# Kernel tuning notes

Hardware: AMD Instinct MI355X
Metric: run time of the kernel (lower is better)

## Reference

```python
import jax, jax.numpy as jnp
import numpy as np

C = 256
CI = C // 2  # inter_channels


def conv1x1(x, w, b):
    # x: [B,C,H,W], w: [O,C], b: [O] -> [B,O,H,W]
    return jnp.einsum('bchw,oc->bohw', x, w) + b[None, :, None, None]


def setup_inputs() -> dict:
    key = jax.random.key(0)
    ks = jax.random.split(key, 9)
    B, H, W = 8, 56, 56
    s = 0.02
    return {
        'x': jax.random.normal(ks[0], (B, C, H, W), dtype=jnp.float32),
        'g_w': jax.random.normal(ks[1], (CI, C), dtype=jnp.float32) * s,
        'g_b': jax.random.normal(ks[2], (CI,), dtype=jnp.float32) * s,
        'theta_w': jax.random.normal(ks[3], (CI, C), dtype=jnp.float32) * s,
        'theta_b': jax.random.normal(ks[4], (CI,), dtype=jnp.float32) * s,
        'phi_w': jax.random.normal(ks[5], (CI, C), dtype=jnp.float32) * s,
        'phi_b': jax.random.normal(ks[6], (CI,), dtype=jnp.float32) * s,
        'W_w': jax.random.normal(ks[7], (C, CI), dtype=jnp.float32) * s,
        'W_b': jax.random.normal(ks[8], (C,), dtype=jnp.float32) * s,
    }


def reference(x, g_w, g_b, theta_w, theta_b, phi_w, phi_b, W_w, W_b):
    B, Cc, H, Wd = x.shape
    N = H * Wd
    g_x = conv1x1(x, g_w, g_b).reshape(B, CI, N).transpose(0, 2, 1)        # [B,N,CI]
    theta_x = conv1x1(x, theta_w, theta_b).reshape(B, CI, N).transpose(0, 2, 1)  # [B,N,CI]
    phi_x = conv1x1(x, phi_w, phi_b).reshape(B, CI, N)                     # [B,CI,N]
    f = jnp.einsum('bnc,bcm->bnm', theta_x, phi_x)                         # [B,N,N]
    attn = jax.nn.softmax(f, axis=-1)
    y = jnp.einsum('bnm,bmc->bnc', attn, g_x)                              # [B,N,CI]
    y = y.transpose(0, 2, 1).reshape(B, CI, H, Wd)                         # [B,CI,H,W]
    z = conv1x1(y, W_w, W_b) + x
    return z
```

## Files before the change

### kernel.cpp

```cpp
#include <hip/hip_runtime.h>

#define NB 8
#define C 256
#define CI 128
#define NPIX 3136
#define NT 64
#define NTILES 49
#define NG 25
#define NSPLIT 4
#define LOG2E 1.44269504f

typedef unsigned short u16;
typedef unsigned int u32;
typedef __bf16 bf16x8 __attribute__((ext_vector_type(8)));
typedef float f32x4 __attribute__((ext_vector_type(4)));
typedef float f32x16 __attribute__((ext_vector_type(16)));

static __device__ __forceinline__ u16 f2b(float f) {
  union { float f; u32 u; } v; v.f = f;
  u32 r = v.u + 0x7FFFu + ((v.u >> 16) & 1u);
  return (u16)(r >> 16);
}
static __device__ __forceinline__ float b2f(u16 v) {
  union { u32 u; float f; } x; x.u = ((u32)v) << 16; return x.f;
}
static __device__ __forceinline__ u32 cvtpk(float lo, float hi) {
  u32 r;
  asm("v_cvt_pk_bf16_f32 %0, %1, %2" : "=v"(r) : "v"(lo), "v"(hi));
  return r;
}
static __device__ __forceinline__ void swap32(u32& x, u32& y) {
  asm("v_permlane32_swap_b32 %0, %1" : "+v"(x), "+v"(y));
}
static __device__ __forceinline__ void gl16(const void* g, void* l) {
  __builtin_amdgcn_global_load_lds(
      (const __attribute__((address_space(1))) u32*)g,
      (__attribute__((address_space(3))) u32*)l, 16, 0, 0);
}

__global__ __launch_bounds__(256) void k0_convert(
    const float* __restrict__ g_w, const float* __restrict__ th_w,
    const float* __restrict__ ph_w, const float* __restrict__ W_w,
    u16* __restrict__ wcat, u16* __restrict__ Wbf) {
  int i = blockIdx.x * 256 + threadIdx.x;
  if (i < 98304) {
    int o = i >> 8, c = i & 255;
    float v = (o < 128) ? g_w[o * 256 + c]
            : (o < 256) ? th_w[(o - 128) * 256 + c] * LOG2E
                        : ph_w[(o - 256) * 256 + c];
    wcat[i] = f2b(v);
  } else {
    int j = i - 98304;
    Wbf[j] = f2b(W_w[j]);
  }
}

__global__ __launch_bounds__(256) void k1_proj(
    const float* __restrict__ x, const float* __restrict__ g_b,
    const float* __restrict__ th_b, const float* __restrict__ ph_b,
    const u16* __restrict__ wcat, u16* __restrict__ thO,
    u16* __restrict__ phO, u16* __restrict__ gO) {
  __shared__ __align__(16) u16 xT[64 * 256];
  char* xTb = reinterpret_cast<char*>(xT);
  int tid = threadIdx.x;
  int b = blockIdx.x / NTILES, nt = blockIdx.x % NTILES;
  int n0 = nt * NT;
  const float* xb = x + (size_t)b * C * NPIX;
  {
    int c0 = tid >> 4, nq = tid & 15;
    for (int k = 0; k < 16; ++k) {
      int c = c0 + 16 * k;
      float4 xv = *reinterpret_cast<const float4*>(xb + (size_t)c * NPIX + n0 + 4 * nq);
      float vals[4] = {xv.x, xv.y, xv.z, xv.w};
#pragma unroll
      for (int j = 0; j < 4; ++j) {
        int row = 4 * nq + j;
        int off = row * 512 + ((((c >> 3) ^ (row & 7))) << 4) + (c & 7) * 2;
        *reinterpret_cast<u16*>(xTb + off) = f2b(vals[j]);
      }
    }
  }
  __syncthreads();
  int wave = tid >> 6, lane = tid & 63;
  int r = 16 * wave + (lane & 15);
  bf16x8 a[8];
#pragma unroll
  for (int kk = 0; kk < 8; ++kk) {
    int ch = 4 * kk + (lane >> 4);
    a[kk] = *reinterpret_cast<const bf16x8*>(xTb + r * 512 + ((ch ^ (r & 7)) << 4));
  }
  for (int os = 0; os < 24; ++os) {
    int o = 16 * os + (lane & 15);
    f32x4 acc = {0.f, 0.f, 0.f, 0.f};
    const u16* wrow = wcat + (size_t)o * 256 + 8 * (lane >> 4);
#pragma unroll
    for (int kk = 0; kk < 8; ++kk) {
      bf16x8 bb = *reinterpret_cast<const bf16x8*>(wrow + 32 * kk);
      acc = __builtin_amdgcn_mfma_f32_16x16x32_bf16(a[kk], bb, acc, 0, 0, 0);
    }
    int p = os >> 3;
    int ol = (os & 7) * 16 + (lane & 15);
    const float* bias = (p == 0) ? g_b : (p == 1) ? th_b : ph_b;
    float bv = bias[ol];
    if (p == 1) bv *= LOG2E;
    int nbase = n0 + 16 * wave + 4 * (lane >> 4);
    if (p == 0) {
      ushort4 pk;
      pk.x = f2b(acc[0] + bv); pk.y = f2b(acc[1] + bv);
      pk.z = f2b(acc[2] + bv); pk.w = f2b(acc[3] + bv);
      *reinterpret_cast<ushort4*>(gO + ((size_t)b * CI + ol) * NPIX + nbase) = pk;
    } else {
      u16* dst = (p == 1) ? thO : phO;
#pragma unroll
      for (int j = 0; j < 4; ++j)
        dst[((size_t)b * NPIX + nbase + j) * CI + ol] = f2b(acc[j] + bv);
    }
  }
}

__global__ __launch_bounds__(256, 2) void k2_attn(
    const u16* __restrict__ th, const u16* __restrict__ ph,
    const u16* __restrict__ gbuf, u16* __restrict__ yp,
    float* __restrict__ lm) {
  __shared__ __align__(16) char lds[65536];
  int tid = threadIdx.x, wave = tid >> 6, lane = tid & 63;
  int h5 = lane >> 5, l31 = lane & 31;
  int bid = blockIdx.x;
  int s = bid & 3, rest = bid >> 2;
  int b = rest / NG, ng = rest % NG;
  int qbase = ng * 128 + wave * 32;
  if (qbase + 32 > NPIX) qbase -= 64;
  int ts = (NTILES * s) >> 2, te = (NTILES * (s + 1)) >> 2;

  bf16x8 bth[8];
  {
    const u16* trow = th + ((size_t)b * NPIX + qbase + l31) * CI;
#pragma unroll
    for (int ks = 0; ks < 8; ++ks)
      bth[ks] = *reinterpret_cast<const bf16x8*>(trow + 16 * ks + 8 * h5);
  }
  float mrun = -1e30f, lrun = 0.f;
  f32x16 yacc[4];
#pragma unroll
  for (int cb = 0; cb < 4; ++cb)
#pragma unroll
    for (int j = 0; j < 16; ++j) yacc[cb][j] = 0.f;

  auto stage = [&](int buf, int mt) {
    int m0 = mt * NT;
    char* phB = lds + buf * 16384;
    char* gB = lds + 32768 + buf * 16384;
#pragma unroll
    for (int c = 0; c < 4; ++c) {
      int call = wave * 4 + c;
      int o = call * 1024 + lane * 16;
      int row = o >> 8, chl = (o >> 4) & 15;
      int chg = chl ^ (row & 7);
      gl16(ph + ((size_t)(b * NPIX + m0 + row)) * CI + chg * 8, phB + call * 1024);
    }
#pragma unroll
    for (int c = 0; c < 4; ++c) {
      int call = wave * 4 + c;
      int o = call * 1024 + lane * 16;
      int ci = o >> 7, chl = (o >> 4) & 7;
      int chg = chl ^ (ci & 7);
      gl16(gbuf + ((size_t)b * CI + ci) * NPIX + m0 + chg * 8, gB + call * 1024);
    }
  };

  stage(0, ts);
  __syncthreads();
  int cur = 0;
  for (int mt = ts; mt < te; ++mt) {
    if (mt + 1 < te) stage(cur ^ 1, mt + 1);
    char* phB = lds + cur * 16384;
    char* gB = lds + 32768 + cur * 16384;
    f32x16 sv0, sv1;
#pragma unroll
    for (int j = 0; j < 16; ++j) { sv0[j] = 0.f; sv1[j] = 0.f; }
    __builtin_amdgcn_s_setprio(1);
#pragma unroll
    for (int ks = 0; ks < 8; ++ks) {
      int chk = 2 * ks + h5;
      int off = l31 * 256 + ((chk ^ (l31 & 7)) << 4);
      bf16x8 a0 = *reinterpret_cast<const bf16x8*>(phB + off);
      bf16x8 a1 = *reinterpret_cast<const bf16x8*>(phB + off + 8192);
      sv0 = __builtin_amdgcn_mfma_f32_32x32x16_bf16(a0, bth[ks], sv0, 0, 0, 0);
      sv1 = __builtin_amdgcn_mfma_f32_32x32x16_bf16(a1, bth[ks], sv1, 0, 0, 0);
    }
    __builtin_amdgcn_s_setprio(0);
    float m8[8];
#pragma unroll
    for (int i = 0; i < 8; ++i)
      m8[i] = fmaxf(fmaxf(sv0[i], sv0[i + 8]), fmaxf(sv1[i], sv1[i + 8]));
    float pmax = fmaxf(fmaxf(fmaxf(m8[0], m8[1]), fmaxf(m8[2], m8[3])),
                       fmaxf(fmaxf(m8[4], m8[5]), fmaxf(m8[6], m8[7])));
    pmax = fmaxf(pmax, __shfl_xor(pmax, 32));
    if (!__all(pmax <= mrun + 11.5f)) {
      float mn = fmaxf(mrun, pmax);
      float corr = exp2f(mrun - mn);
      mrun = mn; lrun *= corr;
      float cr[16];
#pragma unroll
      for (int j = 0; j < 16; ++j) {
        int row = (j & 3) + 8 * (j >> 2) + 4 * h5;
        cr[j] = __shfl(corr, row + 32 * h5);
      }
#pragma unroll
      for (int cb = 0; cb < 4; ++cb)
#pragma unroll
        for (int j = 0; j < 16; ++j) yacc[cb][j] *= cr[j];
    }
#pragma unroll
    for (int j = 0; j < 16; ++j) {
      sv0[j] = exp2f(sv0[j] - mrun);
      sv1[j] = exp2f(sv1[j] - mrun);
    }
    float a0 = 0.f, a1 = 0.f, a2 = 0.f, a3 = 0.f;
#pragma unroll
    for (int i = 0; i < 16; i += 4) {
      a0 += sv0[i] + sv1[i];
      a1 += sv0[i + 1] + sv1[i + 1];
      a2 += sv0[i + 2] + sv1[i + 2];
      a3 += sv0[i + 3] + sv1[i + 3];
    }
    float rs = (a0 + a1) + (a2 + a3);
    rs += __shfl_xor(rs, 32);
    lrun += rs;
    u32 pk[2][4][2];
#pragma unroll
    for (int t = 0; t < 4; ++t) {
      pk[0][t][0] = cvtpk(sv0[4 * t], sv0[4 * t + 1]);
      pk[0][t][1] = cvtpk(sv0[4 * t + 2], sv0[4 * t + 3]);
      pk[1][t][0] = cvtpk(sv1[4 * t], sv1[4 * t + 1]);
      pk[1][t][1] = cvtpk(sv1[4 * t + 2], sv1[4 * t + 3]);
    }
    __builtin_amdgcn_s_setprio(1);
#pragma unroll
    for (int ks = 0; ks < 4; ++ks) {
      int m2 = ks >> 1, t0 = 2 * (ks & 1);
      swap32(pk[m2][t0][0], pk[m2][t0 + 1][0]);
      swap32(pk[m2][t0][1], pk[m2][t0 + 1][1]);
      union { u32 u[4]; bf16x8 v; } f;
      f.u[0] = pk[m2][t0][0]; f.u[1] = pk[m2][t0][1];
      f.u[2] = pk[m2][t0 + 1][0]; f.u[3] = pk[m2][t0 + 1][1];
      int chk = 2 * ks + h5;
#pragma unroll
      for (int cb = 0; cb < 4; ++cb) {
        int ci = 32 * cb + l31;
        bf16x8 gv = *reinterpret_cast<const bf16x8*>(
            gB + ci * 128 + ((chk ^ (ci & 7)) << 4));
        yacc[cb] = __builtin_amdgcn_mfma_f32_32x32x16_bf16(f.v, gv, yacc[cb], 0, 0, 0);
      }
    }
    __builtin_amdgcn_s_setprio(0);
    __syncthreads();
    cur ^= 1;
  }
  u16* ypb = yp + (size_t)(s * NB + b) * NPIX * CI;
#pragma unroll
  for (int cb = 0; cb < 4; ++cb)
#pragma unroll
    for (int j = 0; j < 16; ++j) {
      int n = qbase + (j & 3) + 8 * (j >> 2) + 4 * h5;
      ypb[(size_t)n * CI + 32 * cb + l31] = f2b(yacc[cb][j]);
    }
  if (lane < 32) {
    int n = qbase + l31;
    float* lmb = lm + (size_t)(s * NB + b) * 2 * NPIX;
    lmb[n] = mrun;
    lmb[NPIX + n] = lrun;
  }
}

__global__ __launch_bounds__(256) void k3_out(
    const u16* __restrict__ yp, const float* __restrict__ lm,
    const u16* __restrict__ Wbf, const float* __restrict__ W_b,
    const float* __restrict__ x, float* __restrict__ z) {
  __shared__ __align__(16) u16 yT[64 * 128];
  char* yTb = reinterpret_cast<char*>(yT);
  int tid = threadIdx.x, wave = tid >> 6, lane = tid & 63;
  int b = blockIdx.x / NTILES, nt = blockIdx.x % NTILES;
  int n0 = nt * NT;
#pragma unroll
  for (int i = 0; i < 4; ++i) {
    int qq = tid + i * 256;
    int row = qq >> 4, ch = qq & 15;
    int n = n0 + row;
    float mv[NSPLIT], lv[NSPLIT];
    float M = -1e30f;
#pragma unroll
    for (int s = 0; s < NSPLIT; ++s) {
      const float* lmb = lm + (size_t)(s * NB + b) * 2 * NPIX;
      mv[s] = lmb[n]; lv[s] = lmb[NPIX + n];
      M = fmaxf(M, mv[s]);
    }
    float num[8];
#pragma unroll
    for (int e = 0; e < 8; ++e) num[e] = 0.f;
    float den = 0.f;
#pragma unroll
    for (int s = 0; s < NSPLIT; ++s) {
      float w = exp2f(mv[s] - M);
      den += w * lv[s];
      union { uint4 u4; u16 us[8]; } yv;
      yv.u4 = *reinterpret_cast<const uint4*>(
          yp + (size_t)(s * NB + b) * NPIX * CI + (size_t)n * CI + ch * 8);
#pragma unroll
      for (int e = 0; e < 8; ++e) num[e] += w * b2f(yv.us[e]);
    }
    float inv = 1.f / den;
    union { uint4 u4; u16 us[8]; } ov;
#pragma unroll
    for (int e = 0; e < 8; ++e) ov.us[e] = f2b(num[e] * inv);
    *reinterpret_cast<uint4*>(yTb + row * 256 + ((ch ^ (row & 7)) << 4)) = ov.u4;
  }
  __syncthreads();
  bf16x8 a[4];
  int r = 16 * wave + (lane & 15);
#pragma unroll
  for (int kk = 0; kk < 4; ++kk) {
    int ch = 4 * kk + (lane >> 4);
    a[kk] = *reinterpret_cast<const bf16x8*>(yTb + r * 256 + ((ch ^ (r & 7)) << 4));
  }
  for (int os = 0; os < 16; ++os) {
    int co = 16 * os + (lane & 15);
    f32x4 acc = {0.f, 0.f, 0.f, 0.f};
    const u16* wrow = Wbf + (size_t)co * 128 + 8 * (lane >> 4);
#pragma unroll
    for (int kk = 0; kk < 4; ++kk) {
      bf16x8 bb = *reinterpret_cast<const bf16x8*>(wrow + 32 * kk);
      acc = __builtin_amdgcn_mfma_f32_16x16x32_bf16(a[kk], bb, acc, 0, 0, 0);
    }
    float bw = W_b[co];
    int nb = n0 + 16 * wave + 4 * (lane >> 4);
    size_t off = ((size_t)b * C + co) * NPIX + nb;
    float4 xv = *reinterpret_cast<const float4*>(x + off);
    float4 o;
    o.x = acc[0] + bw + xv.x; o.y = acc[1] + bw + xv.y;
    o.z = acc[2] + bw + xv.z; o.w = acc[3] + bw + xv.w;
    *reinterpret_cast<float4*>(z + off) = o;
  }
}

extern "C" void kernel_launch(void* const* d_in, const int* in_sizes, int n_in,
                              void* d_out, int out_size, void* d_ws, size_t ws_size,
                              hipStream_t stream) {
  const float* x    = (const float*)d_in[0];
  const float* g_w  = (const float*)d_in[1];
  const float* g_b  = (const float*)d_in[2];
  const float* th_w = (const float*)d_in[3];
  const float* th_b = (const float*)d_in[4];
  const float* ph_w = (const float*)d_in[5];
  const float* ph_b = (const float*)d_in[6];
  const float* W_w  = (const float*)d_in[7];
  const float* W_b  = (const float*)d_in[8];
  float* z = (float*)d_out;
  u16* ws = (u16*)d_ws;
  u16* wcat = ws;
  u16* Wbf  = ws + 98304;
  u16* th   = ws + 131072;
  u16* phb  = th + 3211264;
  u16* gbb  = phb + 3211264;
  u16* yp   = gbb + 3211264;
  float* lm = (float*)(ws + 131072 + (size_t)3211264 * 7);
  hipLaunchKernelGGL(k0_convert, dim3(512), dim3(256), 0, stream,
                     g_w, th_w, ph_w, W_w, wcat, Wbf);
  hipLaunchKernelGGL(k1_proj, dim3(NB * NTILES), dim3(256), 0, stream,
                     x, g_b, th_b, ph_b, wcat, th, phb, gbb);
  hipLaunchKernelGGL(k2_attn, dim3(NB * NG * NSPLIT), dim3(256), 0, stream,
                     th, phb, gbb, yp, lm);
  hipLaunchKernelGGL(k3_out, dim3(NB * NTILES), dim3(256), 0, stream,
                     yp, lm, Wbf, W_b, x, z);
}
```

Measured before the change: 157.2 us.

## Halve pixel tiles in projection/output kernels and tighten attention loop sync

The projection and output kernels now use 32-pixel tiles, giving twice as many blocks, with waves split across output channels to raise occupancy and parallelism. In the attention kernel, the phi LDS swizzle now uses 16 XOR patterns instead of 8 to cut bank conflicts. The per-iteration __syncthreads is replaced with explicit vmcnt/lgkmcnt waits plus raw barriers, so the prefetch of the next tile can stay in flight across the barrier. Each weight row is now loaded by more blocks, and the hand-written waitcnt counts must match the number of outstanding loads.

```diff
diff --git a/kernel.cpp b/kernel.cpp
--- a/kernel.cpp
+++ b/kernel.cpp
@@ -7,6 +7,7 @@
 #define NT 64
 #define NTILES 49
 #define NG 25
+#define NROWT 98
 #define NSPLIT 4
 #define LOG2E 1.44269504f
 
@@ -60,16 +61,16 @@
     const float* __restrict__ th_b, const float* __restrict__ ph_b,
     const u16* __restrict__ wcat, u16* __restrict__ thO,
     u16* __restrict__ phO, u16* __restrict__ gO) {
-  __shared__ __align__(16) u16 xT[64 * 256];
+  __shared__ __align__(16) u16 xT[32 * 256];
   char* xTb = reinterpret_cast<char*>(xT);
   int tid = threadIdx.x;
-  int b = blockIdx.x / NTILES, nt = blockIdx.x % NTILES;
-  int n0 = nt * NT;
+  int b = blockIdx.x / NROWT, nt = blockIdx.x % NROWT;
+  int n0 = nt * 32;
   const float* xb = x + (size_t)b * C * NPIX;
   {
-    int c0 = tid >> 4, nq = tid & 15;
-    for (int k = 0; k < 16; ++k) {
-      int c = c0 + 16 * k;
+    int c0 = tid >> 3, nq = tid & 7;
+    for (int k = 0; k < 8; ++k) {
+      int c = c0 + 32 * k;
       float4 xv = *reinterpret_cast<const float4*>(xb + (size_t)c * NPIX + n0 + 4 * nq);
       float vals[4] = {xv.x, xv.y, xv.z, xv.w};
 #pragma unroll
@@ -82,14 +83,15 @@
   }
   __syncthreads();
   int wave = tid >> 6, lane = tid & 63;
-  int r = 16 * wave + (lane & 15);
+  int wq = wave & 1, wo = wave >> 1;
+  int r = 16 * wq + (lane & 15);
   bf16x8 a[8];
 #pragma unroll
   for (int kk = 0; kk < 8; ++kk) {
     int ch = 4 * kk + (lane >> 4);
     a[kk] = *reinterpret_cast<const bf16x8*>(xTb + r * 512 + ((ch ^ (r & 7)) << 4));
   }
-  for (int os = 0; os < 24; ++os) {
+  for (int os = 12 * wo; os < 12 * wo + 12; ++os) {
     int o = 16 * os + (lane & 15);
     f32x4 acc = {0.f, 0.f, 0.f, 0.f};
     const u16* wrow = wcat + (size_t)o * 256 + 8 * (lane >> 4);
@@ -103,7 +105,7 @@
     const float* bias = (p == 0) ? g_b : (p == 1) ? th_b : ph_b;
     float bv = bias[ol];
     if (p == 1) bv *= LOG2E;
-    int nbase = n0 + 16 * wave + 4 * (lane >> 4);
+    int nbase = n0 + 16 * wq + 4 * (lane >> 4);
     if (p == 0) {
       ushort4 pk;
       pk.x = f2b(acc[0] + bv); pk.y = f2b(acc[1] + bv);
@@ -155,7 +157,7 @@
       int call = wave * 4 + c;
       int o = call * 1024 + lane * 16;
       int row = o >> 8, chl = (o >> 4) & 15;
-      int chg = chl ^ (row & 7);
+      int chg = chl ^ (row & 15);
       gl16(ph + ((size_t)(b * NPIX + m0 + row)) * CI + chg * 8, phB + call * 1024);
     }
 #pragma unroll
@@ -169,10 +171,17 @@
   };
 
   stage(0, ts);
-  __syncthreads();
   int cur = 0;
   for (int mt = ts; mt < te; ++mt) {
-    if (mt + 1 < te) stage(cur ^ 1, mt + 1);
+    bool pre = (mt + 1 < te);
+    if (pre) stage(cur ^ 1, mt + 1);
+    if (pre) {
+      asm volatile("s_waitcnt vmcnt(8)" ::: "memory");
+    } else {
+      asm volatile("s_waitcnt vmcnt(0)" ::: "memory");
+    }
+    __builtin_amdgcn_s_barrier();
+    __builtin_amdgcn_sched_barrier(0);
     char* phB = lds + cur * 16384;
     char* gB = lds + 32768 + cur * 16384;
     f32x16 sv0, sv1;
@@ -182,7 +191,7 @@
 #pragma unroll
     for (int ks = 0; ks < 8; ++ks) {
       int chk = 2 * ks + h5;
-      int off = l31 * 256 + ((chk ^ (l31 & 7)) << 4);
+      int off = l31 * 256 + ((chk ^ (l31 & 15)) << 4);
       bf16x8 a0 = *reinterpret_cast<const bf16x8*>(phB + off);
       bf16x8 a1 = *reinterpret_cast<const bf16x8*>(phB + off + 8192);
       sv0 = __builtin_amdgcn_mfma_f32_32x32x16_bf16(a0, bth[ks], sv0, 0, 0, 0);
@@ -254,7 +263,9 @@
       }
     }
     __builtin_amdgcn_s_setprio(0);
-    __syncthreads();
+    __builtin_amdgcn_sched_barrier(0);
+    asm volatile("s_waitcnt lgkmcnt(0)" ::: "memory");
+    __builtin_amdgcn_s_barrier();
     cur ^= 1;
   }
   u16* ypb = yp + (size_t)(s * NB + b) * NPIX * CI;
@@ -277,13 +288,13 @@
     const u16* __restrict__ yp, const float* __restrict__ lm,
     const u16* __restrict__ Wbf, const float* __restrict__ W_b,
     const float* __restrict__ x, float* __restrict__ z) {
-  __shared__ __align__(16) u16 yT[64 * 128];
+  __shared__ __align__(16) u16 yT[32 * 128];
   char* yTb = reinterpret_cast<char*>(yT);
   int tid = threadIdx.x, wave = tid >> 6, lane = tid & 63;
-  int b = blockIdx.x / NTILES, nt = blockIdx.x % NTILES;
-  int n0 = nt * NT;
-#pragma unroll
-  for (int i = 0; i < 4; ++i) {
+  int b = blockIdx.x / NROWT, nt = blockIdx.x % NROWT;
+  int n0 = nt * 32;
+#pragma unroll
+  for (int i = 0; i < 2; ++i) {
     int qq = tid + i * 256;
     int row = qq >> 4, ch = qq & 15;
     int n = n0 + row;
@@ -316,14 +327,15 @@
     *reinterpret_cast<uint4*>(yTb + row * 256 + ((ch ^ (row & 7)) << 4)) = ov.u4;
   }
   __syncthreads();
+  int wq = wave & 1, wo = wave >> 1;
   bf16x8 a[4];
-  int r = 16 * wave + (lane & 15);
+  int r = 16 * wq + (lane & 15);
 #pragma unroll
   for (int kk = 0; kk < 4; ++kk) {
     int ch = 4 * kk + (lane >> 4);
     a[kk] = *reinterpret_cast<const bf16x8*>(yTb + r * 256 + ((ch ^ (r & 7)) << 4));
   }
-  for (int os = 0; os < 16; ++os) {
+  for (int os = 8 * wo; os < 8 * wo + 8; ++os) {
     int co = 16 * os + (lane & 15);
     f32x4 acc = {0.f, 0.f, 0.f, 0.f};
     const u16* wrow = Wbf + (size_t)co * 128 + 8 * (lane >> 4);
@@ -333,7 +345,7 @@
       acc = __builtin_amdgcn_mfma_f32_16x16x32_bf16(a[kk], bb, acc, 0, 0, 0);
     }
     float bw = W_b[co];
-    int nb = n0 + 16 * wave + 4 * (lane >> 4);
+    int nb = n0 + 16 * wq + 4 * (lane >> 4);
     size_t off = ((size_t)b * C + co) * NPIX + nb;
     float4 xv = *reinterpret_cast<const float4*>(x + off);
     float4 o;
@@ -366,10 +378,10 @@
   float* lm = (float*)(ws + 131072 + (size_t)3211264 * 7);
   hipLaunchKernelGGL(k0_convert, dim3(512), dim3(256), 0, stream,
                      g_w, th_w, ph_w, W_w, wcat, Wbf);
-  hipLaunchKernelGGL(k1_proj, dim3(NB * NTILES), dim3(256), 0, stream,
+  hipLaunchKernelGGL(k1_proj, dim3(NB * NROWT), dim3(256), 0, stream,
                      x, g_b, th_b, ph_b, wcat, th, phb, gbb);
   hipLaunchKernelGGL(k2_attn, dim3(NB * NG * NSPLIT), dim3(256), 0, stream,
                      th, phb, gbb, yp, lm);
-  hipLaunchKernelGGL(k3_out, dim3(NB * NTILES), dim3(256), 0, stream,
+  hipLaunchKernelGGL(k3_out, dim3(NB * NROWT), dim3(256), 0, stream,
                      yp, lm, Wbf, W_b, x, z);
 }
```

New measurement: 153.5 us. -2.3%, faster.
